# Optimization experiments

Hardware: AMD Instinct MI355X
Metric: run time of the kernel (lower is better)

## Reference

```python
import jax, jax.numpy as jnp
import numpy as np

D_IN, D, TOPK = 64, 4, 12
SCALE = 1.0 / np.sqrt(np.float32(D_IN))


def setup_inputs() -> dict:
    key = jax.random.key(0)
    kx, kw = jax.random.split(key)
    x = jax.random.normal(kx, (8, 16, 512, D_IN), dtype=jnp.float32)
    flat = jax.random.normal(kw, (2 * D_IN * D,), dtype=jnp.float32)
    return {"x": x, "flat": flat}


def reference(x, flat):
    # x: (N, T, n, d_in); flat holds wk then wq, each (d_in, d)
    wk = flat[: D_IN * D].reshape(D_IN, D)
    wq = flat[D_IN * D :].reshape(D_IN, D)
    N, T, n, _ = x.shape
    k = jnp.einsum("btnc,cd->btnd", x, wk)  # (N,T,n,d)
    q = jnp.einsum("btnc,cd->btnd", x, wq)  # (N,T,n,d)
    # h = (X Wk)(X Wq)^T : h[i,j] = k_i . q_j -> (N,T,n,n)
    h = jnp.einsum("btnd,btmd->btnm", k, q)
    A = jax.nn.softmax(SCALE * h, axis=-1).sum(axis=-2)  # (N,T,n) column score sums
    # argsort descending + slice topk == top_k indices (values sorted descending)
    _, idxs = jax.lax.top_k(A, TOPK)  # (N,T,topk)
    return idxs.reshape(N, T, TOPK, 1)
```

## Files before the change

### kernel.cpp

```cpp
#include <hip/hip_runtime.h>
#include <math.h>

constexpr int kDIn  = 64;
constexpr int kN    = 512;
constexpr int kTopK = 12;
constexpr int kNBt  = 128;
constexpr int kS    = 8;
constexpr int kRows = kN / kS;
#define CEXP 0.18033688f
#define EXP2(v) __builtin_amdgcn_exp2f(v)
#define LOG2F(v) __builtin_amdgcn_logf(v)

#define DOT4(k, q)        fmaf((k).x,(q).x, fmaf((k).y,(q).y, fmaf((k).z,(q).z, (k).w*(q).w)))
#define DOT4A(k, q, add)  fmaf((k).x,(q).x, fmaf((k).y,(q).y, fmaf((k).z,(q).z, fmaf((k).w,(q).w,(add)))))

constexpr size_t kWsFloats = (size_t)kNBt * kS * kN;

__global__ __launch_bounds__(512, 8) void fused_attn_kernel(
    const float* __restrict__ x, const float* __restrict__ flat,
    float* __restrict__ apart)
{
  __shared__ float4 Wk[kDIn];
  __shared__ float4 Wq[kDIn];
  __shared__ float4 Qs[kN];
  __shared__ float4 Ks[kRows];
  __shared__ float2 Pp[kN];
  __shared__ __align__(16) float Cs[kRows];

  const int tid  = threadIdx.x;
  const int p    = blockIdx.x;
  const int xcd  = p & 7;
  const int s    = (p >> 3) & 7;
  const int tile = ((p >> 6) << 3) | xcd;

  if (tid < 64)       Wk[tid]      = reinterpret_cast<const float4*>(flat)[tid];
  else if (tid < 128) Wq[tid - 64] = reinterpret_cast<const float4*>(flat)[tid];
  __syncthreads();

  {
    const float4* xr4 = reinterpret_cast<const float4*>(x + ((size_t)tile * kN + tid) * kDIn);
    float q0=0.f,q1=0.f,q2=0.f,q3=0.f;
    if ((tid >> 6) == s) {
      float k0=0.f,k1=0.f,k2=0.f,k3=0.f;
#pragma unroll
      for (int cc = 0; cc < kDIn / 4; ++cc) {
        float4 xv = xr4[cc];
#pragma unroll
        for (int u = 0; u < 4; ++u) {
          float v = (u==0)?xv.x:(u==1)?xv.y:(u==2)?xv.z:xv.w;
          float4 a = Wk[cc*4+u];
          float4 b = Wq[cc*4+u];
          k0 = fmaf(v, a.x, k0); k1 = fmaf(v, a.y, k1);
          k2 = fmaf(v, a.z, k2); k3 = fmaf(v, a.w, k3);
          q0 = fmaf(v, b.x, q0); q1 = fmaf(v, b.y, q1);
          q2 = fmaf(v, b.z, q2); q3 = fmaf(v, b.w, q3);
        }
      }
      Ks[tid & 63] = make_float4(CEXP*k0, CEXP*k1, CEXP*k2, CEXP*k3);
    } else {
#pragma unroll
      for (int cc = 0; cc < kDIn / 4; ++cc) {
        float4 xv = xr4[cc];
#pragma unroll
        for (int u = 0; u < 4; ++u) {
          float v = (u==0)?xv.x:(u==1)?xv.y:(u==2)?xv.z:xv.w;
          float4 b = Wq[cc*4+u];
          q0 = fmaf(v, b.x, q0); q1 = fmaf(v, b.y, q1);
          q2 = fmaf(v, b.z, q2); q3 = fmaf(v, b.w, q3);
        }
      }
    }
    Qs[tid] = make_float4(q0, q1, q2, q3);
  }
  __syncthreads();

  {
    const float4 k = Ks[tid & 63];
    const float4* qb = &Qs[(tid >> 6) << 6];

    float m = -INFINITY, l0 = 0.f, l1 = 0.f;
#pragma unroll 2
    for (int c = 0; c < kRows; c += 8) {
      float4 qa = qb[c],   qb_ = qb[c+1], qc = qb[c+2], qd = qb[c+3];
      float4 qe = qb[c+4], qf  = qb[c+5], qg = qb[c+6], qh = qb[c+7];
      float h0 = DOT4(k, qa),  h1 = DOT4(k, qb_), h2 = DOT4(k, qc), h3 = DOT4(k, qd);
      float h4 = DOT4(k, qe),  h5 = DOT4(k, qf),  h6 = DOT4(k, qg), h7 = DOT4(k, qh);
      float cm = fmaxf(fmaxf(fmaxf(h0,h1), fmaxf(h2,h3)),
                       fmaxf(fmaxf(h4,h5), fmaxf(h6,h7)));
      if (cm > m) {
        float f = EXP2(m - cm);
        l0 *= f; l1 *= f; m = cm;
      }
      l0 += EXP2(h0 - m); l1 += EXP2(h1 - m);
      l0 += EXP2(h2 - m); l1 += EXP2(h3 - m);
      l0 += EXP2(h4 - m); l1 += EXP2(h5 - m);
      l0 += EXP2(h6 - m); l1 += EXP2(h7 - m);
    }
    Pp[tid] = make_float2(m, l0 + l1);
  }
  __syncthreads();
  if (tid < kRows) {
    float2 p0 = Pp[tid],           p1 = Pp[tid + 64],  p2 = Pp[tid + 128], p3 = Pp[tid + 192];
    float2 p4 = Pp[tid + 256],     p5 = Pp[tid + 320], p6 = Pp[tid + 384], p7 = Pp[tid + 448];
    float m = fmaxf(fmaxf(fmaxf(p0.x,p1.x), fmaxf(p2.x,p3.x)),
                    fmaxf(fmaxf(p4.x,p5.x), fmaxf(p6.x,p7.x)));
    float l = fmaf(p0.y, EXP2(p0.x - m), p1.y * EXP2(p1.x - m)) +
              fmaf(p2.y, EXP2(p2.x - m), p3.y * EXP2(p3.x - m)) +
              fmaf(p4.y, EXP2(p4.x - m), p5.y * EXP2(p5.x - m)) +
              fmaf(p6.y, EXP2(p6.x - m), p7.y * EXP2(p7.x - m));
    Cs[tid] = m + LOG2F(l);
  }
  __syncthreads();

  {
    const float4 q = Qs[tid];
    float a0 = 0.f, a1 = 0.f;
#pragma unroll 4
    for (int i = 0; i < kRows; i += 4) {
      float4 k0 = Ks[i], k1 = Ks[i+1], k2 = Ks[i+2], k3 = Ks[i+3];
      float4 cc = *reinterpret_cast<const float4*>(&Cs[i]);
      a0 += EXP2(DOT4A(q, k0, -cc.x));
      a1 += EXP2(DOT4A(q, k1, -cc.y));
      a0 += EXP2(DOT4A(q, k2, -cc.z));
      a1 += EXP2(DOT4A(q, k3, -cc.w));
    }
    apart[((size_t)tile * kS + s) * kN + tid] = a0 + a1;
  }
}

__global__ __launch_bounds__(64) void topk_kernel(
    const float* __restrict__ apart, int* __restrict__ out)
{
  const int lane = threadIdx.x;
  const int bt   = blockIdx.x;
  const float* P = apart + (size_t)bt * kS * kN;

  float v[8];
  {
    float4 acc0 = make_float4(0.f,0.f,0.f,0.f);
    float4 acc1 = make_float4(0.f,0.f,0.f,0.f);
#pragma unroll
    for (int s = 0; s < kS; ++s) {
      const float4* Ps = reinterpret_cast<const float4*>(P + s * kN);
      float4 u0 = Ps[lane*2], u1 = Ps[lane*2+1];
      acc0.x += u0.x; acc0.y += u0.y; acc0.z += u0.z; acc0.w += u0.w;
      acc1.x += u1.x; acc1.y += u1.y; acc1.z += u1.z; acc1.w += u1.w;
    }
    v[0]=acc0.x; v[1]=acc0.y; v[2]=acc0.z; v[3]=acc0.w;
    v[4]=acc1.x; v[5]=acc1.y; v[6]=acc1.z; v[7]=acc1.w;
  }

  for (int rnd = 0; rnd < kTopK; ++rnd) {
    float bv = v[0];
    int   bi = lane * 8;
#pragma unroll
    for (int r = 1; r < 8; ++r) {
      if (v[r] > bv) { bv = v[r]; bi = lane * 8 + r; }
    }
#pragma unroll
    for (int off = 32; off >= 1; off >>= 1) {
      float ov = __shfl_xor(bv, off);
      int   oi = __shfl_xor(bi, off);
      if (ov > bv || (ov == bv && oi < bi)) { bv = ov; bi = oi; }
    }
    if (lane == 0) out[bt * kTopK + rnd] = bi;
#pragma unroll
    for (int r = 0; r < 8; ++r) {
      if (lane * 8 + r == bi) v[r] = -INFINITY;
    }
  }
}

__global__ __launch_bounds__(512, 1) void sparse_attn_topk_fallback(
    const float* __restrict__ x, const float* __restrict__ flat, int* __restrict__ out)
{
  __shared__ float4 wk4[kDIn];
  __shared__ float4 wq4[kDIn];
  __shared__ float4 Ks[kN];
  __shared__ float4 Qs[kN];
  __shared__ float  Ms[kN];
  __shared__ float  Rl[kN];
  __shared__ float  As[kN];

  const int tid = threadIdx.x;
  const int bt  = blockIdx.x;

  if (tid < 64)       wk4[tid]      = reinterpret_cast<const float4*>(flat)[tid];
  else if (tid < 128) wq4[tid - 64] = reinterpret_cast<const float4*>(flat)[tid];
  __syncthreads();

  const float* xr = x + ((size_t)bt * kN + tid) * kDIn;
  float k0=0.f,k1=0.f,k2=0.f,k3=0.f, q0=0.f,q1=0.f,q2=0.f,q3=0.f;
#pragma unroll
  for (int c = 0; c < kDIn; ++c) {
    float xv = xr[c];
    float4 a = wk4[c];
    float4 b = wq4[c];
    k0 = fmaf(xv, a.x, k0); k1 = fmaf(xv, a.y, k1);
    k2 = fmaf(xv, a.z, k2); k3 = fmaf(xv, a.w, k3);
    q0 = fmaf(xv, b.x, q0); q1 = fmaf(xv, b.y, q1);
    q2 = fmaf(xv, b.z, q2); q3 = fmaf(xv, b.w, q3);
  }
  Ks[tid] = make_float4(k0, k1, k2, k3);
  Qs[tid] = make_float4(q0, q1, q2, q3);
  __syncthreads();

  float m = -INFINITY;
#pragma unroll 8
  for (int j = 0; j < kN; ++j) {
    float4 qj = Qs[j];
    float h = fmaf(k0, qj.x, fmaf(k1, qj.y, fmaf(k2, qj.z, k3 * qj.w)));
    m = fmaxf(m, h);
  }
  float l = 0.f;
#pragma unroll 8
  for (int j = 0; j < kN; ++j) {
    float4 qj = Qs[j];
    float h = fmaf(k0, qj.x, fmaf(k1, qj.y, fmaf(k2, qj.z, k3 * qj.w)));
    l += exp2f(CEXP * (h - m));
  }
  Ms[tid] = m;
  Rl[tid] = 1.0f / l;
  __syncthreads();

  float acc = 0.f;
#pragma unroll 8
  for (int i = 0; i < kN; ++i) {
    float4 ki = Ks[i];
    float h = fmaf(q0, ki.x, fmaf(q1, ki.y, fmaf(q2, ki.z, q3 * ki.w)));
    acc += exp2f(CEXP * (h - Ms[i])) * Rl[i];
  }
  As[tid] = acc;
  __syncthreads();

  if (tid < 64) {
    float v[8];
#pragma unroll
    for (int r = 0; r < 8; ++r) v[r] = As[tid * 8 + r];
    for (int rnd = 0; rnd < kTopK; ++rnd) {
      float bv = v[0];
      int   bi = tid * 8;
#pragma unroll
      for (int r = 1; r < 8; ++r)
        if (v[r] > bv) { bv = v[r]; bi = tid * 8 + r; }
#pragma unroll
      for (int off = 32; off >= 1; off >>= 1) {
        float ov = __shfl_xor(bv, off);
        int   oi = __shfl_xor(bi, off);
        if (ov > bv || (ov == bv && oi < bi)) { bv = ov; bi = oi; }
      }
      if (tid == 0) out[bt * kTopK + rnd] = bi;
#pragma unroll
      for (int r = 0; r < 8; ++r)
        if (tid * 8 + r == bi) v[r] = -INFINITY;
    }
  }
}

extern "C" void kernel_launch(void* const* d_in, const int* in_sizes, int n_in,
                              void* d_out, int out_size, void* d_ws, size_t ws_size,
                              hipStream_t stream) {
  const float* x    = (const float*)d_in[0];
  const float* flat = (const float*)d_in[1];
  int* out = (int*)d_out;
  const int n_bt = in_sizes[0] / (kN * kDIn);

  if (n_bt != kNBt || ws_size < kWsFloats * sizeof(float)) {
    sparse_attn_topk_fallback<<<n_bt, kN, 0, stream>>>(x, flat, out);
    return;
  }
  float* apart = (float*)d_ws;
  fused_attn_kernel<<<kNBt * kS, 512, 0, stream>>>(x, flat, apart);
  topk_kernel      <<<kNBt,       64, 0, stream>>>(apart, out);
}
```

Measured before the change: 43.01 us.

## Halve row splits and register-block attention passes with 4x4 tiles

```diff
diff --git a/kernel.cpp b/kernel.cpp
--- a/kernel.cpp
+++ b/kernel.cpp
@@ -5,7 +5,7 @@
 constexpr int kN    = 512;
 constexpr int kTopK = 12;
 constexpr int kNBt  = 128;
-constexpr int kS    = 8;
+constexpr int kS    = 4;
 constexpr int kRows = kN / kS;
 #define CEXP 0.18033688f
 #define EXP2(v) __builtin_amdgcn_exp2f(v)
@@ -14,9 +14,9 @@
 #define DOT4(k, q)        fmaf((k).x,(q).x, fmaf((k).y,(q).y, fmaf((k).z,(q).z, (k).w*(q).w)))
 #define DOT4A(k, q, add)  fmaf((k).x,(q).x, fmaf((k).y,(q).y, fmaf((k).z,(q).z, fmaf((k).w,(q).w,(add)))))
 
-constexpr size_t kWsFloats = (size_t)kNBt * kS * kN;
-
-__global__ __launch_bounds__(512, 8) void fused_attn_kernel(
+constexpr size_t kWsFloats = (size_t)kNBt * 16 * kN;
+
+__global__ __launch_bounds__(512, 4) void fused_attn_kernel(
     const float* __restrict__ x, const float* __restrict__ flat,
     float* __restrict__ apart)
 {
@@ -24,14 +24,14 @@
   __shared__ float4 Wq[kDIn];
   __shared__ float4 Qs[kN];
   __shared__ float4 Ks[kRows];
-  __shared__ float2 Pp[kN];
+  __shared__ float2 Pp[16 * kRows];
   __shared__ __align__(16) float Cs[kRows];
 
   const int tid  = threadIdx.x;
   const int p    = blockIdx.x;
   const int xcd  = p & 7;
-  const int s    = (p >> 3) & 7;
-  const int tile = ((p >> 6) << 3) | xcd;
+  const int s    = (p >> 3) & 3;
+  const int tile = ((p >> 5) << 3) | xcd;
 
   if (tid < 64)       Wk[tid]      = reinterpret_cast<const float4*>(flat)[tid];
   else if (tid < 128) Wq[tid - 64] = reinterpret_cast<const float4*>(flat)[tid];
@@ -40,7 +40,7 @@
   {
     const float4* xr4 = reinterpret_cast<const float4*>(x + ((size_t)tile * kN + tid) * kDIn);
     float q0=0.f,q1=0.f,q2=0.f,q3=0.f;
-    if ((tid >> 6) == s) {
+    if ((tid >> 7) == s) {
       float k0=0.f,k1=0.f,k2=0.f,k3=0.f;
 #pragma unroll
       for (int cc = 0; cc < kDIn / 4; ++cc) {
@@ -56,7 +56,7 @@
           q2 = fmaf(v, b.z, q2); q3 = fmaf(v, b.w, q3);
         }
       }
-      Ks[tid & 63] = make_float4(CEXP*k0, CEXP*k1, CEXP*k2, CEXP*k3);
+      Ks[tid & 127] = make_float4(CEXP*k0, CEXP*k1, CEXP*k2, CEXP*k3);
     } else {
 #pragma unroll
       for (int cc = 0; cc < kDIn / 4; ++cc) {
@@ -75,56 +75,75 @@
   __syncthreads();
 
   {
-    const float4 k = Ks[tid & 63];
-    const float4* qb = &Qs[(tid >> 6) << 6];
-
-    float m = -INFINITY, l0 = 0.f, l1 = 0.f;
+    const int quad  = tid & 31;
+    const int slice = tid >> 5;
+    const float4 k0 = Ks[quad*4+0], k1 = Ks[quad*4+1];
+    const float4 k2 = Ks[quad*4+2], k3 = Ks[quad*4+3];
+    const float4* qb = &Qs[slice << 5];
+
+    float m0=-INFINITY, m1=-INFINITY, m2=-INFINITY, m3=-INFINITY;
+#pragma unroll 4
+    for (int j = 0; j < 32; ++j) {
+      float4 q = qb[j];
+      m0 = fmaxf(m0, DOT4(k0, q));
+      m1 = fmaxf(m1, DOT4(k1, q));
+      m2 = fmaxf(m2, DOT4(k2, q));
+      m3 = fmaxf(m3, DOT4(k3, q));
+    }
+    float l0=0.f, l1=0.f, l2=0.f, l3=0.f;
+#pragma unroll 4
+    for (int j = 0; j < 32; ++j) {
+      float4 q = qb[j];
+      l0 += EXP2(DOT4A(k0, q, -m0));
+      l1 += EXP2(DOT4A(k1, q, -m1));
+      l2 += EXP2(DOT4A(k2, q, -m2));
+      l3 += EXP2(DOT4A(k3, q, -m3));
+    }
+    float4* pp4 = reinterpret_cast<float4*>(&Pp[slice * kRows + quad*4]);
+    pp4[0] = make_float4(m0, l0, m1, l1);
+    pp4[1] = make_float4(m2, l2, m3, l3);
+  }
+  __syncthreads();
+
+  if (tid < kRows) {
+    float m = -INFINITY;
+    float2 pr[16];
+#pragma unroll
+    for (int sl = 0; sl < 16; ++sl) {
+      pr[sl] = Pp[sl * kRows + tid];
+      m = fmaxf(m, pr[sl].x);
+    }
+    float l = 0.f;
+#pragma unroll
+    for (int sl = 0; sl < 16; ++sl) l += pr[sl].y * EXP2(pr[sl].x - m);
+    Cs[tid] = m + LOG2F(l);
+  }
+  __syncthreads();
+
+  {
+    const int cq = tid & 127;
+    const int rs = tid >> 7;
+    const float4 q0 = Qs[cq*4+0], q1 = Qs[cq*4+1];
+    const float4 q2 = Qs[cq*4+2], q3 = Qs[cq*4+3];
+    const float4* kb = &Ks[rs << 5];
+    const float4* cb = reinterpret_cast<const float4*>(&Cs[rs << 5]);
+
+    float a0=0.f, a1=0.f, a2=0.f, a3=0.f;
 #pragma unroll 2
-    for (int c = 0; c < kRows; c += 8) {
-      float4 qa = qb[c],   qb_ = qb[c+1], qc = qb[c+2], qd = qb[c+3];
-      float4 qe = qb[c+4], qf  = qb[c+5], qg = qb[c+6], qh = qb[c+7];
-      float h0 = DOT4(k, qa),  h1 = DOT4(k, qb_), h2 = DOT4(k, qc), h3 = DOT4(k, qd);
-      float h4 = DOT4(k, qe),  h5 = DOT4(k, qf),  h6 = DOT4(k, qg), h7 = DOT4(k, qh);
-      float cm = fmaxf(fmaxf(fmaxf(h0,h1), fmaxf(h2,h3)),
-                       fmaxf(fmaxf(h4,h5), fmaxf(h6,h7)));
-      if (cm > m) {
-        float f = EXP2(m - cm);
-        l0 *= f; l1 *= f; m = cm;
-      }
-      l0 += EXP2(h0 - m); l1 += EXP2(h1 - m);
-      l0 += EXP2(h2 - m); l1 += EXP2(h3 - m);
-      l0 += EXP2(h4 - m); l1 += EXP2(h5 - m);
-      l0 += EXP2(h6 - m); l1 += EXP2(h7 - m);
-    }
-    Pp[tid] = make_float2(m, l0 + l1);
-  }
-  __syncthreads();
-  if (tid < kRows) {
-    float2 p0 = Pp[tid],           p1 = Pp[tid + 64],  p2 = Pp[tid + 128], p3 = Pp[tid + 192];
-    float2 p4 = Pp[tid + 256],     p5 = Pp[tid + 320], p6 = Pp[tid + 384], p7 = Pp[tid + 448];
-    float m = fmaxf(fmaxf(fmaxf(p0.x,p1.x), fmaxf(p2.x,p3.x)),
-                    fmaxf(fmaxf(p4.x,p5.x), fmaxf(p6.x,p7.x)));
-    float l = fmaf(p0.y, EXP2(p0.x - m), p1.y * EXP2(p1.x - m)) +
-              fmaf(p2.y, EXP2(p2.x - m), p3.y * EXP2(p3.x - m)) +
-              fmaf(p4.y, EXP2(p4.x - m), p5.y * EXP2(p5.x - m)) +
-              fmaf(p6.y, EXP2(p6.x - m), p7.y * EXP2(p7.x - m));
-    Cs[tid] = m + LOG2F(l);
-  }
-  __syncthreads();
-
-  {
-    const float4 q = Qs[tid];
-    float a0 = 0.f, a1 = 0.f;
-#pragma unroll 4
-    for (int i = 0; i < kRows; i += 4) {
-      float4 k0 = Ks[i], k1 = Ks[i+1], k2 = Ks[i+2], k3 = Ks[i+3];
-      float4 cc = *reinterpret_cast<const float4*>(&Cs[i]);
-      a0 += EXP2(DOT4A(q, k0, -cc.x));
-      a1 += EXP2(DOT4A(q, k1, -cc.y));
-      a0 += EXP2(DOT4A(q, k2, -cc.z));
-      a1 += EXP2(DOT4A(q, k3, -cc.w));
-    }
-    apart[((size_t)tile * kS + s) * kN + tid] = a0 + a1;
+    for (int ii = 0; ii < 8; ++ii) {
+      float4 cc = cb[ii];
+      float4 ka = kb[ii*4+0], kb_ = kb[ii*4+1], kc = kb[ii*4+2], kd = kb[ii*4+3];
+      a0 += EXP2(DOT4A(q0, ka, -cc.x));  a1 += EXP2(DOT4A(q1, ka, -cc.x));
+      a2 += EXP2(DOT4A(q2, ka, -cc.x));  a3 += EXP2(DOT4A(q3, ka, -cc.x));
+      a0 += EXP2(DOT4A(q0, kb_, -cc.y)); a1 += EXP2(DOT4A(q1, kb_, -cc.y));
+      a2 += EXP2(DOT4A(q2, kb_, -cc.y)); a3 += EXP2(DOT4A(q3, kb_, -cc.y));
+      a0 += EXP2(DOT4A(q0, kc, -cc.z));  a1 += EXP2(DOT4A(q1, kc, -cc.z));
+      a2 += EXP2(DOT4A(q2, kc, -cc.z));  a3 += EXP2(DOT4A(q3, kc, -cc.z));
+      a0 += EXP2(DOT4A(q0, kd, -cc.w));  a1 += EXP2(DOT4A(q1, kd, -cc.w));
+      a2 += EXP2(DOT4A(q2, kd, -cc.w));  a3 += EXP2(DOT4A(q3, kd, -cc.w));
+    }
+    reinterpret_cast<float4*>(apart + ((size_t)(tile*4 + s) * 4 + rs) * kN)[cq] =
+        make_float4(a0, a1, a2, a3);
   }
 }
 
@@ -133,15 +152,15 @@
 {
   const int lane = threadIdx.x;
   const int bt   = blockIdx.x;
-  const float* P = apart + (size_t)bt * kS * kN;
+  const float* P = apart + (size_t)bt * 16 * kN;
 
   float v[8];
   {
     float4 acc0 = make_float4(0.f,0.f,0.f,0.f);
     float4 acc1 = make_float4(0.f,0.f,0.f,0.f);
 #pragma unroll
-    for (int s = 0; s < kS; ++s) {
-      const float4* Ps = reinterpret_cast<const float4*>(P + s * kN);
+    for (int sl = 0; sl < 16; ++sl) {
+      const float4* Ps = reinterpret_cast<const float4*>(P + sl * kN);
       float4 u0 = Ps[lane*2], u1 = Ps[lane*2+1];
       acc0.x += u0.x; acc0.y += u0.y; acc0.z += u0.z; acc0.w += u0.w;
       acc1.x += u1.x; acc1.y += u1.y; acc1.z += u1.z; acc1.w += u1.w;
```

Result: faster. 40.38 us (-6.1%).
